# Optimization experiments

Measured on AMD Instinct MI355X. Metric: run time of the kernel, lower is better.

## Reference

```python
import jax, jax.numpy as jnp
import numpy as np

BS, FEAT, EMB, MEM, VOCAB, T = 256, 2048, 512, 1024, 10000, 32
PAD_IDX = 0

def setup_inputs() -> dict:
    key = jax.random.key(0)
    ks = jax.random.split(key, 16)
    s = lambda fan_in: 1.0 / np.sqrt(fan_in)
    return {
        'feature': jax.random.normal(ks[0], (BS, FEAT), jnp.float32),
        'caption': jax.random.randint(ks[1], (BS, T), 0, VOCAB, jnp.int64),
        'length': jax.random.randint(ks[2], (BS,), 0, T, jnp.int64),
        'W_init_h': jax.random.uniform(ks[3], (MEM, FEAT), jnp.float32, -s(FEAT), s(FEAT)),
        'b_init_h': jnp.zeros((MEM,), jnp.float32),
        'W_init_c': jax.random.uniform(ks[4], (MEM, FEAT), jnp.float32, -s(FEAT), s(FEAT)),
        'b_init_c': jnp.zeros((MEM,), jnp.float32),
        'emb_table': jax.random.normal(ks[5], (VOCAB, EMB), jnp.float32) * 0.1,
        'W_ih': jax.random.uniform(ks[6], (4 * MEM, EMB), jnp.float32, -s(MEM), s(MEM)),
        'b_ih': jnp.zeros((4 * MEM,), jnp.float32),
        'W_hh': jax.random.uniform(ks[7], (4 * MEM, MEM), jnp.float32, -s(MEM), s(MEM)),
        'b_hh': jnp.zeros((4 * MEM,), jnp.float32),
        'W_out': jax.random.uniform(ks[8], (VOCAB, MEM), jnp.float32, -s(MEM), s(MEM)),
        'b_out': jnp.zeros((VOCAB,), jnp.float32),
    }


def _forward(feature, caption, W_init_h, b_init_h, W_init_c, b_init_c,
             emb_table, W_ih, b_ih, W_hh, b_hh, W_out, b_out):
    h0 = feature @ W_init_h.T + b_init_h            # (bs, mem)
    c0 = feature @ W_init_c.T + b_init_c
    cap_emb = emb_table[caption]                     # (bs, T, emb)
    # teacher forcing (ss_prob=0): inputs are cap_emb[:, 0:T-1]
    xs = jnp.transpose(cap_emb[:, :-1, :], (1, 0, 2))  # (T-1, bs, emb)

    def step(carry, x):
        h, c = carry
        gates = x @ W_ih.T + b_ih + h @ W_hh.T + b_hh  # (bs, 4*mem)
        i, f, g, o = jnp.split(gates, 4, axis=-1)      # PyTorch order i,f,g,o
        c_new = jax.nn.sigmoid(f) * c + jax.nn.sigmoid(i) * jnp.tanh(g)
        h_new = jax.nn.sigmoid(o) * jnp.tanh(c_new)
        logits = h_new @ W_out.T + b_out               # dropout_p=0 -> identity
        return (h_new, c_new), logits

    _, logits = jax.lax.scan(step, (h0, c0), xs)       # (T-1, bs, vocab)
    logits = jnp.transpose(logits, (1, 0, 2))          # (bs, T-1, vocab)

    targets = caption[:, 1:]                            # (bs, T-1)
    logp = jax.nn.log_softmax(logits, axis=-1)
    nll = -jnp.take_along_axis(logp, targets[..., None], axis=-1)[..., 0]
    mask = (targets != PAD_IDX).astype(logits.dtype)
    loss = jnp.sum(nll * mask) / jnp.maximum(jnp.sum(mask), 1.0)
    return loss


def reference(feature, caption, length, W_init_h, b_init_h, W_init_c, b_init_c,
              emb_table, W_ih, b_ih, W_hh, b_hh, W_out, b_out):
    return _forward(feature, caption, W_init_h, b_init_h, W_init_c, b_init_c,
                    emb_table, W_ih, b_ih, W_hh, b_hh, W_out, b_out)
```

## Files before the change

kernel.cpp:

```cpp
#include <hip/hip_runtime.h>
#include <math.h>

#define BS_    256
#define FEAT_  2048
#define EMB_   512
#define MEM_   1024
#define VOCAB_ 10000
#define TT_    32
#define NSTEP  31
#define VT_    128
#define NTV_   79
#define MROWS_ 7936
#define PAD_   40
#define SP_    80

typedef unsigned short u16;
typedef __bf16 bf16x8 __attribute__((ext_vector_type(8)));
typedef float  f32x4  __attribute__((ext_vector_type(4)));
typedef u16    u16x8  __attribute__((ext_vector_type(8)));
typedef u16    u16x4  __attribute__((ext_vector_type(4)));
typedef bf16x8 __attribute__((may_alias)) bf16x8_ma;
typedef u16x8  __attribute__((may_alias)) u16x8_ma;
typedef u16x4  __attribute__((may_alias)) u16x4_ma;
typedef float4 __attribute__((may_alias)) float4_ma;

__device__ __forceinline__ u16 f2bf(float f) {
  unsigned u = __float_as_uint(f);
  u += 0x7FFFu + ((u >> 16) & 1u);
  return (u16)(u >> 16);
}

__device__ __forceinline__ void async16(const void* g, void* s) {
  __builtin_amdgcn_global_load_lds((const __attribute__((address_space(1))) void*)g,
                                   (__attribute__((address_space(3))) void*)s, 16, 0, 0);
}

__device__ __forceinline__ float redsum16(float v) {
#pragma unroll
  for (int m = 1; m < 16; m <<= 1) v += __shfl_xor(v, m, 64);
  return v;
}
__device__ __forceinline__ float sigmoidf_(float x) { return 1.0f / (1.0f + __expf(-x)); }
__device__ __forceinline__ float tanhf_(float x) {
  float e = __expf(2.0f * x);
  return 1.0f - 2.0f / (e + 1.0f);
}

__global__ __launch_bounds__(256) void cvt_bf16_k(const float* __restrict__ in,
                                                  u16* __restrict__ out, int n4) {
  int i = blockIdx.x * 256 + threadIdx.x;
  if (i >= n4) return;
  float4 v = ((const float4_ma*)in)[i];
  u16x4 o = { f2bf(v.x), f2bf(v.y), f2bf(v.z), f2bf(v.w) };
  *(u16x4_ma*)(out + (size_t)i * 4) = o;
}

__global__ __launch_bounds__(128) void cvt_permute_k(
    const float* __restrict__ W_ih, const float* __restrict__ W_hh,
    const float* __restrict__ b_ih, const float* __restrict__ b_hh,
    u16* __restrict__ WPih, u16* __restrict__ WPhh, float* __restrict__ biasP) {
  int r = blockIdx.x, tid = threadIdx.x;
  int u = r >> 2, g = r & 3, s = g * 1024 + u;
  {
    float4 v = *(const float4_ma*)(W_ih + (size_t)s * EMB_ + tid * 4);
    u16x4 o = { f2bf(v.x), f2bf(v.y), f2bf(v.z), f2bf(v.w) };
    *(u16x4_ma*)(WPih + (size_t)r * EMB_ + tid * 4) = o;
  }
#pragma unroll
  for (int h = 0; h < 2; ++h) {
    int idx = h * 512 + tid * 4;
    float4 v = *(const float4_ma*)(W_hh + (size_t)s * MEM_ + idx);
    u16x4 o = { f2bf(v.x), f2bf(v.y), f2bf(v.z), f2bf(v.w) };
    *(u16x4_ma*)(WPhh + (size_t)r * MEM_ + idx) = o;
  }
  if (tid == 0) biasP[r] = b_ih[s] + b_hh[s];
}

__global__ __launch_bounds__(256) void gather_x_k(const float* __restrict__ emb,
                                                  const int* __restrict__ caption,
                                                  u16* __restrict__ X) {
  int i = blockIdx.x * 256 + threadIdx.x;
  int e4 = (i & 127) * 4;
  int b  = (i >> 7) & 255;
  int t  = i >> 15;
  int cap = caption[b * TT_ + t];
  float4 v = *(const float4_ma*)(emb + (size_t)cap * EMB_ + e4);
  u16x4 o = { f2bf(v.x), f2bf(v.y), f2bf(v.z), f2bf(v.w) };
  *(u16x4_ma*)(X + ((size_t)(t * 256 + b) * EMB_ + e4)) = o;
}

__global__ __launch_bounds__(256) void gemm_nt_bias_k(
    const float* __restrict__ A, const float* __restrict__ B,
    const float* __restrict__ bias, float* __restrict__ C, u16* __restrict__ Cb,
    int M, int N, int K) {
  __shared__ float As[16][65];
  __shared__ float Bs[16][65];
  int tid = threadIdx.x;
  int bx = blockIdx.x, by = blockIdx.y;
  int tx = tid & 15, ty = tid >> 4;
  float acc[4][4] = {};
  for (int k0 = 0; k0 < K; k0 += 16) {
#pragma unroll
    for (int i = 0; i < 4; ++i) {
      int idx = tid + i * 256;
      As[idx & 15][idx >> 4] = A[(size_t)(by * 64 + (idx >> 4)) * K + k0 + (idx & 15)];
    }
#pragma unroll
    for (int i = 0; i < 4; ++i) {
      int idx = tid + i * 256;
      Bs[idx & 15][idx >> 4] = B[(size_t)(bx * 64 + (idx >> 4)) * K + k0 + (idx & 15)];
    }
    __syncthreads();
#pragma unroll
    for (int kk = 0; kk < 16; ++kk) {
      float a[4], b[4];
#pragma unroll
      for (int i = 0; i < 4; ++i) a[i] = As[kk][ty * 4 + i];
#pragma unroll
      for (int j = 0; j < 4; ++j) b[j] = Bs[kk][tx * 4 + j];
#pragma unroll
      for (int i = 0; i < 4; ++i)
#pragma unroll
        for (int j = 0; j < 4; ++j) acc[i][j] += a[i] * b[j];
    }
    __syncthreads();
  }
#pragma unroll
  for (int i = 0; i < 4; ++i) {
    int gm = by * 64 + ty * 4 + i;
#pragma unroll
    for (int j = 0; j < 4; ++j) {
      int gn = bx * 64 + tx * 4 + j;
      float v = acc[i][j] + bias[gn];
      if (C)  C[(size_t)gm * N + gn] = v;
      if (Cb) Cb[(size_t)gm * N + gn] = f2bf(v);
    }
  }
}

__global__ __launch_bounds__(256) void mfma_init_k(
    const u16* __restrict__ A, const u16* __restrict__ Bw,
    const float* __restrict__ bias, u16* __restrict__ outB, float* __restrict__ outF) {
  __shared__ __align__(16) u16 sA[2][64 * PAD_];
  __shared__ __align__(16) u16 sB[2][64 * PAD_];
  const int tid = threadIdx.x;
  const int m0 = blockIdx.y * 64, n0 = blockIdx.x * 64;
  const int l = tid & 63, wid = tid >> 6;
  const int wm = (wid & 1) * 32, wn = (wid >> 1) * 32;
  const int q = l >> 4, ln = l & 15;
  const int srow = tid >> 2, scol = (tid & 3) * 8;
  const u16* Ar = A + (size_t)(m0 + srow) * FEAT_ + scol;
  const u16* Br = Bw + (size_t)(n0 + srow) * FEAT_ + scol;

  f32x4 acc[2][2];
  const f32x4 z = {0.f, 0.f, 0.f, 0.f};
  acc[0][0] = z; acc[0][1] = z; acc[1][0] = z; acc[1][1] = z;

  u16x8 ra = *(const u16x8_ma*)Ar;
  u16x8 rb = *(const u16x8_ma*)Br;
  int p = 0;
  for (int it = 0; it < FEAT_ / 32; ++it) {
    *(u16x8_ma*)(sA[p] + srow * PAD_ + scol) = ra;
    *(u16x8_ma*)(sB[p] + srow * PAD_ + scol) = rb;
    __syncthreads();
    if (it + 1 < FEAT_ / 32) {
      ra = *(const u16x8_ma*)(Ar + (it + 1) * 32);
      rb = *(const u16x8_ma*)(Br + (it + 1) * 32);
    }
    bf16x8 a0 = *(const bf16x8_ma*)(sA[p] + (wm + ln) * PAD_ + q * 8);
    bf16x8 a1 = *(const bf16x8_ma*)(sA[p] + (wm + 16 + ln) * PAD_ + q * 8);
    bf16x8 b0 = *(const bf16x8_ma*)(sB[p] + (wn + ln) * PAD_ + q * 8);
    bf16x8 b1 = *(const bf16x8_ma*)(sB[p] + (wn + 16 + ln) * PAD_ + q * 8);
    acc[0][0] = __builtin_amdgcn_mfma_f32_16x16x32_bf16(a0, b0, acc[0][0], 0, 0, 0);
    acc[0][1] = __builtin_amdgcn_mfma_f32_16x16x32_bf16(a0, b1, acc[0][1], 0, 0, 0);
    acc[1][0] = __builtin_amdgcn_mfma_f32_16x16x32_bf16(a1, b0, acc[1][0], 0, 0, 0);
    acc[1][1] = __builtin_amdgcn_mfma_f32_16x16x32_bf16(a1, b1, acc[1][1], 0, 0, 0);
    p ^= 1;
  }
#pragma unroll
  for (int i = 0; i < 2; ++i)
#pragma unroll
    for (int j = 0; j < 2; ++j)
#pragma unroll
      for (int r = 0; r < 4; ++r) {
        int row = m0 + wm + i * 16 + q * 4 + r;
        int col = n0 + wn + j * 16 + ln;
        float v = acc[i][j][r] + bias[col];
        if (outB) outB[(size_t)row * MEM_ + col] = f2bf(v);
        if (outF) outF[(size_t)row * MEM_ + col] = v;
      }
}

__global__ __launch_bounds__(256) void lstm_step_k(
    const u16* __restrict__ Xt, const u16* __restrict__ Hin,
    u16* __restrict__ Hout,
    const u16* __restrict__ WPih, const u16* __restrict__ WPhh,
    const float* __restrict__ biasP, float* __restrict__ c) {
  __shared__ __align__(16) u16 sA[2][64 * SP_];
  __shared__ __align__(16) u16 sB[2][64 * SP_];
  __shared__ __align__(16) float sG[64 * 68];
  const int tid = threadIdx.x;
  const int b = blockIdx.x;
  const int m0 = (b >> 6) * 64, nt = b & 63;
  const int l = tid & 63, wid = tid >> 6;
  const int wm = (wid & 1) * 32, wn = (wid >> 1) * 32;
  const int q = l >> 4, ln = l & 15;
  const int srow = tid >> 2, scol = (tid & 3) * 8;

  const u16* aX = Xt  + (size_t)(m0 + srow) * EMB_ + scol;
  const u16* aH = Hin + (size_t)(m0 + srow) * MEM_ + scol;
  const u16* bX = WPih + (size_t)(nt * 64 + srow) * EMB_ + scol;
  const u16* bH = WPhh + (size_t)(nt * 64 + srow) * MEM_ + scol;

  const float bj0 = biasP[nt * 64 + wn + ln];
  const float bj1 = biasP[nt * 64 + wn + 16 + ln];

  f32x4 acc[2][2];
  const f32x4 z = {0.f, 0.f, 0.f, 0.f};
  acc[0][0] = z; acc[0][1] = z; acc[1][0] = z; acc[1][1] = z;

  u16x8 rA[2][2], rB[2][2];
#pragma unroll
  for (int s = 0; s < 2; ++s)
#pragma unroll
    for (int cc = 0; cc < 2; ++cc) {
      int k = s * 64 + cc * 32;
      rA[s][cc] = *(const u16x8_ma*)(aX + k);
      rB[s][cc] = *(const u16x8_ma*)(bX + k);
    }

  for (int it = 0; it < 24; ++it) {
    const int s = it & 1;
#pragma unroll
    for (int cc = 0; cc < 2; ++cc) {
      *(u16x8_ma*)(sA[s] + srow * SP_ + scol + 32 * cc) = rA[s][cc];
      *(u16x8_ma*)(sB[s] + srow * SP_ + scol + 32 * cc) = rB[s][cc];
    }
    __syncthreads();
    if (it + 2 < 24) {
#pragma unroll
      for (int cc = 0; cc < 2; ++cc) {
        int k = (it + 2) * 64 + cc * 32;
        if (k < EMB_) {
          rA[s][cc] = *(const u16x8_ma*)(aX + k);
          rB[s][cc] = *(const u16x8_ma*)(bX + k);
        } else {
          rA[s][cc] = *(const u16x8_ma*)(aH + (k - EMB_));
          rB[s][cc] = *(const u16x8_ma*)(bH + (k - EMB_));
        }
      }
    }
#pragma unroll
    for (int kk = 0; kk < 2; ++kk) {
      bf16x8 a0 = *(const bf16x8_ma*)(sA[s] + (wm + ln) * SP_ + kk * 32 + q * 8);
      bf16x8 a1 = *(const bf16x8_ma*)(sA[s] + (wm + 16 + ln) * SP_ + kk * 32 + q * 8);
      bf16x8 b0 = *(const bf16x8_ma*)(sB[s] + (wn + ln) * SP_ + kk * 32 + q * 8);
      bf16x8 b1 = *(const bf16x8_ma*)(sB[s] + (wn + 16 + ln) * SP_ + kk * 32 + q * 8);
      acc[0][0] = __builtin_amdgcn_mfma_f32_16x16x32_bf16(a0, b0, acc[0][0], 0, 0, 0);
      acc[0][1] = __builtin_amdgcn_mfma_f32_16x16x32_bf16(a0, b1, acc[0][1], 0, 0, 0);
      acc[1][0] = __builtin_amdgcn_mfma_f32_16x16x32_bf16(a1, b0, acc[1][0], 0, 0, 0);
      acc[1][1] = __builtin_amdgcn_mfma_f32_16x16x32_bf16(a1, b1, acc[1][1], 0, 0, 0);
    }
  }

#pragma unroll
  for (int i = 0; i < 2; ++i)
#pragma unroll
    for (int j = 0; j < 2; ++j)
#pragma unroll
      for (int r = 0; r < 4; ++r)
        sG[(wm + i * 16 + q * 4 + r) * 68 + wn + j * 16 + ln] =
            acc[i][j][r] + (j ? bj1 : bj0);
  __syncthreads();

  {
    const int prow = tid >> 2, u0 = (tid & 3) * 4;
    const float* gRow = sG + prow * 68 + u0 * 4;
    float* cp = c + (size_t)(m0 + prow) * MEM_ + nt * 16 + u0;
    float4 cv = *(const float4_ma*)cp;
    float cva[4] = {cv.x, cv.y, cv.z, cv.w};
    u16x4 hv;
    float cna[4];
#pragma unroll
    for (int k = 0; k < 4; ++k) {
      float4 g4 = *(const float4_ma*)(gRow + k * 4);
      float cvn = sigmoidf_(g4.y) * cva[k] + sigmoidf_(g4.x) * tanhf_(g4.z);
      cna[k] = cvn;
      hv[k] = f2bf(sigmoidf_(g4.w) * tanhf_(cvn));
    }
    float4 cn = {cna[0], cna[1], cna[2], cna[3]};
    *(float4_ma*)cp = cn;
    *(u16x4_ma*)(Hout + (size_t)(m0 + prow) * MEM_ + nt * 16 + u0) = hv;
  }
}

__device__ __forceinline__ void logits_decode(int bid, int& vt, int& mt) {
  int xcd = bid & 7, s = bid >> 3;
  vt = s >> 3;
  mt = xcd * 8 + (s & 7);
}

__global__ __launch_bounds__(256) void mfma_logits_k(
    const u16* __restrict__ H, const u16* __restrict__ WoutB,
    const float* __restrict__ bout, const int* __restrict__ caption,
    float* __restrict__ psum, float* __restrict__ tlog) {
  __shared__ __align__(16) u16 sA[2][128 * PAD_];
  __shared__ __align__(16) u16 sB[2][128 * PAD_];
  const int tid = threadIdx.x;
  int vt, mt;
  logits_decode(blockIdx.x, vt, mt);
  if (mt >= 62) return;
  const int n0 = vt * VT_, m0 = mt * 128;
  const int l = tid & 63, wid = tid >> 6;
  const int wm = (wid & 1) * 64, wn = (wid >> 1) * 64;
  const int q = l >> 4, ln = l & 15;

  f32x4 acc[4][4];
  const f32x4 z = {0.f, 0.f, 0.f, 0.f};
#pragma unroll
  for (int i = 0; i < 4; ++i)
#pragma unroll
    for (int j = 0; j < 4; ++j) acc[i][j] = z;

  int arow[2], acol[2], brow[2];
#pragma unroll
  for (int r = 0; r < 2; ++r) {
    int idx = tid + r * 256;
    arow[r] = idx >> 2;
    acol[r] = (idx & 3) * 8;
    int gr = n0 + arow[r];
    brow[r] = (gr > VOCAB_ - 1) ? (VOCAB_ - 1) : gr;
  }

  u16x8 ra[2], rb[2];
#pragma unroll
  for (int r = 0; r < 2; ++r) {
    ra[r] = *(const u16x8_ma*)(H + (size_t)(m0 + arow[r]) * MEM_ + acol[r]);
    rb[r] = *(const u16x8_ma*)(WoutB + (size_t)brow[r] * MEM_ + acol[r]);
  }
  int p = 0;
  for (int it = 0; it < 32; ++it) {
#pragma unroll
    for (int r = 0; r < 2; ++r) {
      *(u16x8_ma*)(sA[p] + arow[r] * PAD_ + acol[r]) = ra[r];
      *(u16x8_ma*)(sB[p] + arow[r] * PAD_ + acol[r]) = rb[r];
    }
    __syncthreads();
    if (it + 1 < 32) {
      int k0 = (it + 1) * 32;
#pragma unroll
      for (int r = 0; r < 2; ++r) {
        ra[r] = *(const u16x8_ma*)(H + (size_t)(m0 + arow[r]) * MEM_ + k0 + acol[r]);
        rb[r] = *(const u16x8_ma*)(WoutB + (size_t)brow[r] * MEM_ + k0 + acol[r]);
      }
    }
    bf16x8 a[4], b[4];
#pragma unroll
    for (int i = 0; i < 4; ++i) a[i] = *(const bf16x8_ma*)(sA[p] + (wm + i * 16 + ln) * PAD_ + q * 8);
#pragma unroll
    for (int j = 0; j < 4; ++j) b[j] = *(const bf16x8_ma*)(sB[p] + (wn + j * 16 + ln) * PAD_ + q * 8);
#pragma unroll
    for (int i = 0; i < 4; ++i)
#pragma unroll
      for (int j = 0; j < 4; ++j)
        acc[i][j] = __builtin_amdgcn_mfma_f32_16x16x32_bf16(a[i], b[j], acc[i][j], 0, 0, 0);
    __syncthreads();
    p ^= 1;
  }

  float* eS = (float*)sA;
  float* eT = eS + 256;
  const int half = wid >> 1;

  int colj[4]; float bj[4];
#pragma unroll
  for (int j = 0; j < 4; ++j) {
    colj[j] = n0 + wn + j * 16 + ln;
    bj[j] = (colj[j] < VOCAB_) ? bout[colj[j]] : 0.f;
  }
#pragma unroll
  for (int i = 0; i < 4; ++i) {
#pragma unroll
    for (int r = 0; r < 4; ++r) {
      const int rloc = wm + i * 16 + q * 4 + r;
      const int trow = m0 + rloc;
      const int tgt = caption[(trow & 255) * TT_ + (trow >> 8) + 1];
      float s = 0.f, tv = 0.f;
#pragma unroll
      for (int j = 0; j < 4; ++j) {
        if (colj[j] < VOCAB_) {
          float v = acc[i][j][r] + bj[j];
          s += __expf(v);
          if (colj[j] == tgt) tv += v;
        }
      }
      s = redsum16(s);
      tv = redsum16(tv);
      if (ln == 0) {
        eS[rloc * 2 + half] = s;
        eT[rloc * 2 + half] = tv;
      }
    }
  }
  __syncthreads();
  if (tid < 128) {
    int trow = m0 + tid;
    psum[(size_t)trow * NTV_ + vt] = eS[tid * 2] + eS[tid * 2 + 1];
    int tgt = caption[(trow & 255) * TT_ + (trow >> 8) + 1];
    if (tgt >= n0 && tgt < n0 + VT_) tlog[trow] = eT[tid * 2] + eT[tid * 2 + 1];
  }
}

__global__ __launch_bounds__(256) void mfma_logits_conv_k(
    const u16* __restrict__ H, const float* __restrict__ WoutF,
    const float* __restrict__ bout, const int* __restrict__ caption,
    float* __restrict__ psum, float* __restrict__ tlog) {
  __shared__ __align__(16) char smem[16384];
  u16* sA = (u16*)smem;
  u16* sB = (u16*)(smem + 8192);
  const int tid = threadIdx.x;
  int vt, mt;
  logits_decode(blockIdx.x, vt, mt);
  if (mt >= 62) return;
  const int n0 = vt * VT_, m0 = mt * 128;
  const int l = tid & 63, wid = tid >> 6;
  const int wm = (wid & 1) * 64, wn = (wid >> 1) * 64;
  const int q = l >> 4, ln = l & 15;
  f32x4 acc[4][4];
  const f32x4 z = {0.f, 0.f, 0.f, 0.f};
#pragma unroll
  for (int i = 0; i < 4; ++i)
#pragma unroll
    for (int j = 0; j < 4; ++j) acc[i][j] = z;
  const int srow = tid >> 2, scol = (tid & 3) * 8;
  int brow[2];
#pragma unroll
  for (int r = 0; r < 2; ++r) {
    int gr = n0 + srow + r * 64;
    brow[r] = (gr > VOCAB_ - 1) ? (VOCAB_ - 1) : gr;
  }
  for (int k0 = 0; k0 < MEM_; k0 += 32) {
#pragma unroll
    for (int r = 0; r < 2; ++r)
      async16(H + (size_t)(m0 + srow + r * 64) * MEM_ + k0 + scol,
              sA + (srow + r * 64) * 32 + scol);
#pragma unroll
    for (int r = 0; r < 2; ++r) {
      const float* g = WoutF + (size_t)brow[r] * MEM_ + k0 + scol;
      float4 v0 = *(const float4_ma*)g;
      float4 v1 = *(const float4_ma*)(g + 4);
      u16x8 o = { f2bf(v0.x), f2bf(v0.y), f2bf(v0.z), f2bf(v0.w),
                  f2bf(v1.x), f2bf(v1.y), f2bf(v1.z), f2bf(v1.w) };
      *(u16x8_ma*)(sB + (srow + r * 64) * 32 + scol) = o;
    }
    __syncthreads();
    bf16x8 a[4], b[4];
#pragma unroll
    for (int i = 0; i < 4; ++i) a[i] = *(const bf16x8_ma*)(sA + (wm + i * 16 + ln) * 32 + q * 8);
#pragma unroll
    for (int j = 0; j < 4; ++j) b[j] = *(const bf16x8_ma*)(sB + (wn + j * 16 + ln) * 32 + q * 8);
#pragma unroll
    for (int i = 0; i < 4; ++i)
#pragma unroll
      for (int j = 0; j < 4; ++j)
        acc[i][j] = __builtin_amdgcn_mfma_f32_16x16x32_bf16(a[i], b[j], acc[i][j], 0, 0, 0);
    __syncthreads();
  }
  float* eS = (float*)smem;
  float* eT = eS + 256;
  const int half = wid >> 1;
  int colj[4]; float bj[4];
#pragma unroll
  for (int j = 0; j < 4; ++j) {
    colj[j] = n0 + wn + j * 16 + ln;
    bj[j] = (colj[j] < VOCAB_) ? bout[colj[j]] : 0.f;
  }
#pragma unroll
  for (int i = 0; i < 4; ++i) {
#pragma unroll
    for (int r = 0; r < 4; ++r) {
      const int rloc = wm + i * 16 + q * 4 + r;
      const int trow = m0 + rloc;
      const int tgt = caption[(trow & 255) * TT_ + (trow >> 8) + 1];
      float s = 0.f, tv = 0.f;
#pragma unroll
      for (int j = 0; j < 4; ++j) {
        if (colj[j] < VOCAB_) {
          float v = acc[i][j][r] + bj[j];
          s += __expf(v);
          if (colj[j] == tgt) tv += v;
        }
      }
      s = redsum16(s);
      tv = redsum16(tv);
      if (ln == 0) { eS[rloc * 2 + half] = s; eT[rloc * 2 + half] = tv; }
    }
  }
  __syncthreads();
  if (tid < 128) {
    int trow = m0 + tid;
    psum[(size_t)trow * NTV_ + vt] = eS[tid * 2] + eS[tid * 2 + 1];
    int tgt = caption[(trow & 255) * TT_ + (trow >> 8) + 1];
    if (tgt >= n0 && tgt < n0 + VT_) tlog[trow] = eT[tid * 2] + eT[tid * 2 + 1];
  }
}

__global__ __launch_bounds__(256) void combine_k(
    const float* __restrict__ psum, const float* __restrict__ tlog,
    const int* __restrict__ caption, float* __restrict__ accum) {
  int r = blockIdx.x * 256 + threadIdx.x;
  if (r >= MROWS_) return;
  const float* ps = psum + (size_t)r * NTV_;
  float s = 0.f;
  for (int j = 0; j < NTV_; ++j) s += ps[j];
  float nll = __logf(s) - tlog[r];
  int tgt = caption[(r & 255) * TT_ + (r >> 8) + 1];
  if (tgt != 0) {
    atomicAdd(&accum[0], nll);
    atomicAdd(&accum[1], 1.f);
  }
}

__global__ void zero_words_k(unsigned* buf) {
  buf[threadIdx.x] = 0u;
}

__global__ void finalize_k(const float* __restrict__ accum, float* __restrict__ out) {
  out[0] = accum[0] / fmaxf(accum[1], 1.0f);
}

extern "C" void kernel_launch(void* const* d_in, const int* in_sizes, int n_in,
                              void* d_out, int out_size, void* d_ws, size_t ws_size,
                              hipStream_t stream) {
  (void)in_sizes; (void)n_in; (void)out_size;
  const float* feature  = (const float*)d_in[0];
  const int*   caption  = (const int*)d_in[1];
  const float* W_init_h = (const float*)d_in[3];
  const float* b_init_h = (const float*)d_in[4];
  const float* W_init_c = (const float*)d_in[5];
  const float* b_init_c = (const float*)d_in[6];
  const float* emb      = (const float*)d_in[7];
  const float* W_ih     = (const float*)d_in[8];
  const float* b_ih     = (const float*)d_in[9];
  const float* W_hh     = (const float*)d_in[10];
  const float* b_hh     = (const float*)d_in[11];
  const float* W_out    = (const float*)d_in[12];
  const float* b_out    = (const float*)d_in[13];
  float* out = (float*)d_out;

  char* p = (char*)d_ws;
  u16* WPih = (u16*)p;       p += (size_t)4096 * 512 * 2;
  u16* WPhh = (u16*)p;       p += (size_t)4096 * 1024 * 2;
  float* biasP = (float*)p;  p += (size_t)4096 * 4;
  u16* Xall = (u16*)p;       p += (size_t)NSTEP * 256 * 512 * 2;
  u16* Hall = (u16*)p;       p += (size_t)32 * 256 * 1024 * 2;
  float* c0 = (float*)p;     p += (size_t)256 * 1024 * 4;
  float* psum = (float*)p;   p += (size_t)MROWS_ * NTV_ * 4;
  float* tlog = (float*)p;   p += (size_t)MROWS_ * 4;
  unsigned* syncbuf = (unsigned*)p; p += 256;
  u16* WoutB = (u16*)p;      p += (size_t)VOCAB_ * 1024 * 2;
  size_t woutEnd = (size_t)(p - (char*)d_ws);
  u16* featB = (u16*)p;      p += (size_t)256 * 2048 * 2;
  u16* WinitHB = (u16*)p;    p += (size_t)1024 * 2048 * 2;
  u16* WinitCB = (u16*)p;    p += (size_t)1024 * 2048 * 2;
  size_t initEnd = (size_t)(p - (char*)d_ws);

  bool haveWoutB = (ws_size >= woutEnd);
  bool haveInitB = (ws_size >= initEnd);

  float* accum = (float*)syncbuf;

  dim3 blk(256);
  zero_words_k<<<1, 64, 0, stream>>>(syncbuf);
  cvt_permute_k<<<4096, 128, 0, stream>>>(W_ih, W_hh, b_ih, b_hh, WPih, WPhh, biasP);
  gather_x_k<<<3968, blk, 0, stream>>>(emb, caption, Xall);
  if (haveWoutB) cvt_bf16_k<<<10000, blk, 0, stream>>>(W_out, WoutB, 2560000);

  if (haveInitB) {
    cvt_bf16_k<<<512, blk, 0, stream>>>(feature, featB, 131072);
    cvt_bf16_k<<<2048, blk, 0, stream>>>(W_init_h, WinitHB, 524288);
    cvt_bf16_k<<<2048, blk, 0, stream>>>(W_init_c, WinitCB, 524288);
    dim3 gi(16, 4);
    mfma_init_k<<<gi, blk, 0, stream>>>(featB, WinitHB, b_init_h, Hall, nullptr);
    mfma_init_k<<<gi, blk, 0, stream>>>(featB, WinitCB, b_init_c, nullptr, c0);
  } else {
    dim3 gi(16, 4);
    gemm_nt_bias_k<<<gi, blk, 0, stream>>>(feature, W_init_h, b_init_h, nullptr, Hall,
                                           BS_, MEM_, FEAT_);
    gemm_nt_bias_k<<<gi, blk, 0, stream>>>(feature, W_init_c, b_init_c, c0, nullptr,
                                           BS_, MEM_, FEAT_);
  }

  for (int t = 0; t < NSTEP; ++t) {
    lstm_step_k<<<256, blk, 0, stream>>>(Xall + (size_t)t * BS_ * EMB_,
                                         Hall + (size_t)t * BS_ * MEM_,
                                         Hall + (size_t)(t + 1) * BS_ * MEM_,
                                         WPih, WPhh, biasP, c0);
  }

  const int LGRID = 8 * 8 * NTV_;
  if (haveWoutB)
    mfma_logits_k<<<LGRID, blk, 0, stream>>>(Hall + (size_t)BS_ * MEM_, WoutB,
                                             b_out, caption, psum, tlog);
  else
    mfma_logits_conv_k<<<LGRID, blk, 0, stream>>>(Hall + (size_t)BS_ * MEM_, W_out,
                                                  b_out, caption, psum, tlog);

  combine_k<<<31, blk, 0, stream>>>(psum, tlog, caption, accum);
  finalize_k<<<1, 1, 0, stream>>>(accum, out);
}
```

Before: 770.7 us.

## Use async global-to-LDS loads in logits GEMM and write target logit directly

The logits GEMM kernel drops its register-staged double-buffered LDS loads and uses async16 global-to-LDS copies into a single unpadded buffer, with a sync before compute. This halves LDS use and cuts staging registers, which may raise occupancy, but removes the overlap between the next tile's loads and the MFMAs and may add bank conflicts. In both logits kernels the target-logit reduction through LDS is replaced by a direct global store from the lane holding the matching column. The SP_ padding constant for another kernel also shrinks from 80 to 72.

```diff
diff --git a/kernel.cpp b/kernel.cpp
--- a/kernel.cpp
+++ b/kernel.cpp
@@ -12,7 +12,7 @@
 #define NTV_   79
 #define MROWS_ 7936
 #define PAD_   40
-#define SP_    80
+#define SP_    72
 
 typedef unsigned short u16;
 typedef __bf16 bf16x8 __attribute__((ext_vector_type(8)));
@@ -304,8 +304,8 @@
     const u16* __restrict__ H, const u16* __restrict__ WoutB,
     const float* __restrict__ bout, const int* __restrict__ caption,
     float* __restrict__ psum, float* __restrict__ tlog) {
-  __shared__ __align__(16) u16 sA[2][128 * PAD_];
-  __shared__ __align__(16) u16 sB[2][128 * PAD_];
+  __shared__ __align__(16) u16 sA[128 * 32];
+  __shared__ __align__(16) u16 sB[128 * 32];
   const int tid = threadIdx.x;
   int vt, mt;
   logits_decode(blockIdx.x, vt, mt);
@@ -322,54 +322,41 @@
 #pragma unroll
     for (int j = 0; j < 4; ++j) acc[i][j] = z;
 
-  int arow[2], acol[2], brow[2];
+  const int srow = tid >> 2, scol = (tid & 3) * 8;
+  int brow[2];
 #pragma unroll
   for (int r = 0; r < 2; ++r) {
-    int idx = tid + r * 256;
-    arow[r] = idx >> 2;
-    acol[r] = (idx & 3) * 8;
-    int gr = n0 + arow[r];
+    int gr = n0 + srow + r * 64;
     brow[r] = (gr > VOCAB_ - 1) ? (VOCAB_ - 1) : gr;
   }
-
-  u16x8 ra[2], rb[2];
-#pragma unroll
-  for (int r = 0; r < 2; ++r) {
-    ra[r] = *(const u16x8_ma*)(H + (size_t)(m0 + arow[r]) * MEM_ + acol[r]);
-    rb[r] = *(const u16x8_ma*)(WoutB + (size_t)brow[r] * MEM_ + acol[r]);
-  }
-  int p = 0;
-  for (int it = 0; it < 32; ++it) {
+  const u16* aSrc[2] = { H + (size_t)(m0 + srow) * MEM_ + scol,
+                         H + (size_t)(m0 + srow + 64) * MEM_ + scol };
+  const u16* bSrc[2] = { WoutB + (size_t)brow[0] * MEM_ + scol,
+                         WoutB + (size_t)brow[1] * MEM_ + scol };
+  u16* aDst[2] = { sA + srow * 32 + scol, sA + (srow + 64) * 32 + scol };
+  u16* bDst[2] = { sB + srow * 32 + scol, sB + (srow + 64) * 32 + scol };
+
+  for (int k0 = 0; k0 < MEM_; k0 += 32) {
 #pragma unroll
     for (int r = 0; r < 2; ++r) {
-      *(u16x8_ma*)(sA[p] + arow[r] * PAD_ + acol[r]) = ra[r];
-      *(u16x8_ma*)(sB[p] + arow[r] * PAD_ + acol[r]) = rb[r];
-    }
-    __syncthreads();
-    if (it + 1 < 32) {
-      int k0 = (it + 1) * 32;
-#pragma unroll
-      for (int r = 0; r < 2; ++r) {
-        ra[r] = *(const u16x8_ma*)(H + (size_t)(m0 + arow[r]) * MEM_ + k0 + acol[r]);
-        rb[r] = *(const u16x8_ma*)(WoutB + (size_t)brow[r] * MEM_ + k0 + acol[r]);
-      }
-    }
+      async16(aSrc[r] + k0, aDst[r]);
+      async16(bSrc[r] + k0, bDst[r]);
+    }
+    __syncthreads();
     bf16x8 a[4], b[4];
 #pragma unroll
-    for (int i = 0; i < 4; ++i) a[i] = *(const bf16x8_ma*)(sA[p] + (wm + i * 16 + ln) * PAD_ + q * 8);
-#pragma unroll
-    for (int j = 0; j < 4; ++j) b[j] = *(const bf16x8_ma*)(sB[p] + (wn + j * 16 + ln) * PAD_ + q * 8);
+    for (int i = 0; i < 4; ++i) a[i] = *(const bf16x8_ma*)(sA + (wm + i * 16 + ln) * 32 + q * 8);
+#pragma unroll
+    for (int j = 0; j < 4; ++j) b[j] = *(const bf16x8_ma*)(sB + (wn + j * 16 + ln) * 32 + q * 8);
 #pragma unroll
     for (int i = 0; i < 4; ++i)
 #pragma unroll
       for (int j = 0; j < 4; ++j)
         acc[i][j] = __builtin_amdgcn_mfma_f32_16x16x32_bf16(a[i], b[j], acc[i][j], 0, 0, 0);
     __syncthreads();
-    p ^= 1;
   }
 
   float* eS = (float*)sA;
-  float* eT = eS + 256;
   const int half = wid >> 1;
 
   int colj[4]; float bj[4];
@@ -385,29 +372,23 @@
       const int rloc = wm + i * 16 + q * 4 + r;
       const int trow = m0 + rloc;
       const int tgt = caption[(trow & 255) * TT_ + (trow >> 8) + 1];
-      float s = 0.f, tv = 0.f;
+      float s = 0.f;
 #pragma unroll
       for (int j = 0; j < 4; ++j) {
         if (colj[j] < VOCAB_) {
           float v = acc[i][j][r] + bj[j];
           s += __expf(v);
-          if (colj[j] == tgt) tv += v;
+          if (colj[j] == tgt) tlog[trow] = v;
         }
       }
       s = redsum16(s);
-      tv = redsum16(tv);
-      if (ln == 0) {
-        eS[rloc * 2 + half] = s;
-        eT[rloc * 2 + half] = tv;
-      }
+      if (ln == 0) eS[rloc * 2 + half] = s;
     }
   }
   __syncthreads();
   if (tid < 128) {
     int trow = m0 + tid;
     psum[(size_t)trow * NTV_ + vt] = eS[tid * 2] + eS[tid * 2 + 1];
-    int tgt = caption[(trow & 255) * TT_ + (trow >> 8) + 1];
-    if (tgt >= n0 && tgt < n0 + VT_) tlog[trow] = eT[tid * 2] + eT[tid * 2 + 1];
   }
 }
 
@@ -467,7 +448,6 @@
     __syncthreads();
   }
   float* eS = (float*)smem;
-  float* eT = eS + 256;
   const int half = wid >> 1;
   int colj[4]; float bj[4];
 #pragma unroll
@@ -482,26 +462,23 @@
       const int rloc = wm + i * 16 + q * 4 + r;
       const int trow = m0 + rloc;
       const int tgt = caption[(trow & 255) * TT_ + (trow >> 8) + 1];
-      float s = 0.f, tv = 0.f;
+      float s = 0.f;
 #pragma unroll
       for (int j = 0; j < 4; ++j) {
         if (colj[j] < VOCAB_) {
           float v = acc[i][j][r] + bj[j];
           s += __expf(v);
-          if (colj[j] == tgt) tv += v;
+          if (colj[j] == tgt) tlog[trow] = v;
         }
       }
       s = redsum16(s);
-      tv = redsum16(tv);
-      if (ln == 0) { eS[rloc * 2 + half] = s; eT[rloc * 2 + half] = tv; }
+      if (ln == 0) eS[rloc * 2 + half] = s;
     }
   }
   __syncthreads();
   if (tid < 128) {
     int trow = m0 + tid;
     psum[(size_t)trow * NTV_ + vt] = eS[tid * 2] + eS[tid * 2 + 1];
-    int tgt = caption[(trow & 255) * TT_ + (trow >> 8) + 1];
-    if (tgt >= n0 && tgt < n0 + VT_) tlog[trow] = eT[tid * 2] + eT[tid * 2 + 1];
   }
 }
 
```

Measured after the change: 765.2 us. About the same (-0.7%).
